# Optimization experiments

Hardware: AMD Instinct MI355X
Metric: run time of the kernel (lower is better)

Reference implementation:

```python
import jax, jax.numpy as jnp
import numpy as np

BUCKET = 64      # bucket_size
N_HASHES = 8
HEADS = 8
EMB = 256
DH = EMB // HEADS  # 32, per-head dim
SELF_ATTN_VAL = -5e4  # TOKEN_SELF_ATTN_VALUE in reformer-pytorch


def haar_dwt2_per(x):
    # one-level 2D haar DWT, periodization mode. x: [B,C,H,W] (H,W even)
    B, C, H, W = x.shape
    x = x.reshape(B, C, H // 2, 2, W // 2, 2)
    a = x[:, :, :, 0, :, 0]
    b = x[:, :, :, 0, :, 1]
    c = x[:, :, :, 1, :, 0]
    d = x[:, :, :, 1, :, 1]
    ll = (a + b + c + d) * 0.5
    lh = (a - b + c - d) * 0.5  # high-pass along W
    hl = (a + b - c - d) * 0.5  # high-pass along H
    hh = (a - b - c + d) * 0.5
    return ll, lh, hl, hh


def maxpool_3s2p1(x):
    # MaxPool2d(kernel=3, stride=2, padding=1)
    return jax.lax.reduce_window(x, -jnp.inf, jax.lax.max,
                                 (1, 1, 3, 3), (1, 1, 2, 2),
                                 ((0, 0), (0, 0), (1, 1), (1, 1)))


def _look_one_back(a):
    # concat each chunk with the previous chunk (wrap-around), along axis 2
    prev = jnp.concatenate([a[:, -1:], a[:, :-1]], axis=1)
    return jnp.concatenate([a, prev], axis=2)


def lsh_attention(qk, v, rotations):
    # qk, v: [bh, t, d]; rotations: [d, n_hashes, n_buckets//2]
    bh, t, d = qk.shape
    n_buckets = t // BUCKET
    # --- hash ---
    rotated = jnp.einsum('btf,fhi->bhti', qk, rotations)        # [bh,nh,t,nb/2]
    rotated = jnp.concatenate([rotated, -rotated], axis=-1)     # [bh,nh,t,nb]
    buckets = jnp.argmax(rotated, axis=-1)                      # [bh,nh,t]
    offsets = (jnp.arange(N_HASHES) * n_buckets)[None, :, None]
    buckets = (buckets + offsets).reshape(bh, -1)               # [bh, nh*t]
    # --- sort tokens by bucket ---
    ticker = jnp.arange(N_HASHES * t)
    bat = t * buckets + (ticker % t)[None, :]
    sticker = jnp.argsort(bat, axis=-1)                         # stable sort
    undo = jnp.argsort(sticker, axis=-1)
    st = sticker % t
    sqk = jnp.take_along_axis(qk, st[..., None], axis=1)
    sv = jnp.take_along_axis(v, st[..., None], axis=1)
    nc = N_HASHES * n_buckets
    bq_t = st.reshape(bh, nc, BUCKET)
    bqk = sqk.reshape(bh, nc, BUCKET, d)
    bv = sv.reshape(bh, nc, BUCKET, d)
    bq = bqk
    norm = jnp.linalg.norm(bqk, axis=-1, keepdims=True)
    bk = bqk / jnp.maximum(norm, 1e-6)                          # make_unit_length
    bk = _look_one_back(bk)
    bv = _look_one_back(bv)
    bkv_t = _look_one_back(bq_t[..., None])[..., 0]
    # --- bucketed attention ---
    dots = jnp.einsum('bnie,bnje->bnij', bq, bk) * (d ** -0.5)  # [bh,nc,64,128]
    self_mask = bq_t[:, :, :, None] == bkv_t[:, :, None, :]
    dots = jnp.where(self_mask, SELF_ATTN_VAL, dots)
    lse = jax.scipy.special.logsumexp(dots, axis=-1, keepdims=True)
    probs = jnp.exp(dots - lse)
    bo = jnp.einsum('bnij,bnje->bnie', probs, bv)
    so = bo.reshape(bh, -1, d)
    slog = lse.reshape(bh, -1)
    # --- unsort and combine hash rounds ---
    o = jnp.take_along_axis(so, undo[..., None], axis=1).reshape(bh, N_HASHES, t, d)
    logits = jnp.take_along_axis(slog, undo, axis=1).reshape(bh, N_HASHES, t, 1)
    w = jnp.exp(logits - jax.scipy.special.logsumexp(logits, axis=1, keepdims=True))
    return jnp.sum(o * w, axis=1)                               # [bh, t, d]


def setup_inputs() -> dict:
    key = jax.random.key(0)
    ks = jax.random.split(key, 6)
    B, C, H, W = 16, 128, 32, 32
    scale = 1.0 / np.sqrt(EMB)
    return {
        'x': jax.random.normal(ks[0], (B, C, H, W), dtype=jnp.float32),
        'w_qk': jax.random.normal(ks[1], (EMB, EMB), dtype=jnp.float32) * scale,
        'w_v': jax.random.normal(ks[2], (EMB, EMB), dtype=jnp.float32) * scale,
        'w_out': jax.random.normal(ks[3], (EMB, EMB), dtype=jnp.float32) * scale,
        'b_out': jnp.zeros((EMB,), dtype=jnp.float32),
        'rotations': jax.random.normal(ks[4], (DH, N_HASHES, 5), dtype=jnp.float32),
    }


def reference(x, w_qk, w_v, w_out, b_out, rotations):
    B = x.shape[0]
    x_spatial = maxpool_3s2p1(x)                      # [B,C,16,16]
    ll, lh, hl, hh = haar_dwt2_per(x)                 # each [B,C,16,16]
    xc = jnp.concatenate([x_spatial, ll, lh, hl, hh], axis=1)  # [B,5C,16,16]
    _, N, Hh, Ww = xc.shape
    tokens = xc.reshape(B, N, Hh * Ww)                # [B, 640, 256]
    qk = tokens @ w_qk
    v = tokens @ w_v
    qkh = qk.reshape(B, N, HEADS, DH).transpose(0, 2, 1, 3).reshape(B * HEADS, N, DH)
    vh = v.reshape(B, N, HEADS, DH).transpose(0, 2, 1, 3).reshape(B * HEADS, N, DH)
    o = lsh_attention(qkh, vh, rotations)
    o = o.reshape(B, HEADS, N, DH).transpose(0, 2, 1, 3).reshape(B, N, EMB)
    out = o @ w_out + b_out
    return out.reshape(B, N, Hh, Ww)
```

## Files before the change

### kernel.cpp

```cpp
#include <hip/hip_runtime.h>
#include <math.h>

#define B_     16
#define CIN_   128
#define NTOK_  640
#define PSP_   256
#define EMB_   256
#define HEADS_ 8
#define DH_    32
#define BH_    128
#define NH_    8
#define NBK_   10
#define NC_    80
#define TOTROWS_ 10240
#define SORTLEN_ 5120
#define VSTRIDE 136
#define OCSTR  264

typedef __attribute__((ext_vector_type(8))) short short8;
typedef __attribute__((ext_vector_type(4))) short short4v;
typedef __attribute__((ext_vector_type(4))) float f32x4;

__device__ __forceinline__ unsigned bf16r(float f) {
  return (__float_as_uint(f) + 0x8000u) >> 16;
}

__device__ __forceinline__ unsigned cvt_pk_bf16(float a, float b) {
  unsigned r;
  asm("v_cvt_pk_bf16_f32 %0, %1, %2" : "=v"(r) : "v"(a), "v"(b));
  return r;
}

__global__ __launch_bounds__(256) void k_tokens(const float* __restrict__ x,
                                                float* __restrict__ tok,
                                                const float* __restrict__ wv,
                                                const float* __restrict__ wo,
                                                unsigned short* __restrict__ wtv,
                                                unsigned short* __restrict__ wto) {
  if (blockIdx.x < 256) {
    int idx = blockIdx.x * 256 + threadIdx.x;
    int n = idx >> 8, k = idx & 255;
    wtv[idx] = (unsigned short)bf16r(wv[k * 256 + n]);
    wto[idx] = (unsigned short)bf16r(wo[k * 256 + n]);
  }
  int tid = blockIdx.x * 256 + threadIdx.x;
  int p  = tid & 255;
  int bc = tid >> 8;
  int i = p >> 4, j = p & 15;
  const float* xp = x + (size_t)bc * 1024;
  int r0 = i * 2, c0 = j * 2;

  float mx = -3.4e38f;
  #pragma unroll
  for (int dr = -1; dr <= 1; dr++) {
    int r = r0 + dr;
    if (r < 0 || r >= 32) continue;
    #pragma unroll
    for (int dc = -1; dc <= 1; dc++) {
      int cc = c0 + dc;
      if (cc < 0 || cc >= 32) continue;
      mx = fmaxf(mx, xp[r * 32 + cc]);
    }
  }
  float a  = xp[r0 * 32 + c0];
  float bv = xp[r0 * 32 + c0 + 1];
  float cv = xp[(r0 + 1) * 32 + c0];
  float dv = xp[(r0 + 1) * 32 + c0 + 1];
  float ll = (a + bv + cv + dv) * 0.5f;
  float lh = (a - bv + cv - dv) * 0.5f;
  float hl = (a + bv - cv - dv) * 0.5f;
  float hh = (a - bv - cv + dv) * 0.5f;

  int b = bc >> 7, c = bc & 127;
  float* tb = tok + (size_t)b * NTOK_ * PSP_ + p;
  tb[(size_t)(c      ) * PSP_] = mx;
  tb[(size_t)(c + 128) * PSP_] = ll;
  tb[(size_t)(c + 256) * PSP_] = lh;
  tb[(size_t)(c + 384) * PSP_] = hl;
  tb[(size_t)(c + 512) * PSP_] = hh;
}

__global__ __launch_bounds__(256) void k_gemm_qv(const float* __restrict__ A,
                                                 const float* __restrict__ Wq,
                                                 const unsigned short* __restrict__ WTv,
                                                 float* __restrict__ C,
                                                 unsigned short* __restrict__ Cb,
                                                 unsigned short* __restrict__ Cv) {
  __shared__ float As[64][68];
  __shared__ float Bs[64][64];
  int tid = threadIdx.x;

  if (blockIdx.x < 640) {
    int bx = blockIdx.x;
    int row0 = (bx >> 2) * 64, col0 = (bx & 3) * 64;
    int tx = tid & 15, ty = tid >> 4;
    float acc[4][4] = {};

    int lrow = tid >> 2, lkq = tid & 3;
    int bkr = tid >> 4, bcq = tid & 15;

    for (int k0 = 0; k0 < 256; k0 += 64) {
      float4 va[4], vb4[4];
      #pragma unroll
      for (int i = 0; i < 4; i++) {
        va[i]  = *(const float4*)(&A[(size_t)(row0 + lrow) * 256 + k0 + i * 16 + 4 * lkq]);
        vb4[i] = *(const float4*)(&Wq[(size_t)(k0 + i * 16 + bkr) * 256 + col0 + 4 * bcq]);
      }
      __syncthreads();
      #pragma unroll
      for (int i = 0; i < 4; i++) {
        As[i * 16 + 4 * lkq + 0][lrow] = va[i].x;
        As[i * 16 + 4 * lkq + 1][lrow] = va[i].y;
        As[i * 16 + 4 * lkq + 2][lrow] = va[i].z;
        As[i * 16 + 4 * lkq + 3][lrow] = va[i].w;
        *(float4*)(&Bs[i * 16 + bkr][4 * bcq]) = vb4[i];
      }
      __syncthreads();
      #pragma unroll
      for (int k = 0; k < 64; k++) {
        const float4 b4 = *(const float4*)(&Bs[k][4 * tx]);
        const float4 a4 = *(const float4*)(&As[k][4 * ty]);
        float ar[4] = {a4.x, a4.y, a4.z, a4.w};
        #pragma unroll
        for (int r = 0; r < 4; r++) {
          acc[r][0] += ar[r] * b4.x; acc[r][1] += ar[r] * b4.y;
          acc[r][2] += ar[r] * b4.z; acc[r][3] += ar[r] * b4.w;
        }
      }
    }
    #pragma unroll
    for (int r = 0; r < 4; r++) {
      float4 o;
      o.x = acc[r][0]; o.y = acc[r][1]; o.z = acc[r][2]; o.w = acc[r][3];
      size_t off = (size_t)(row0 + 4 * ty + r) * 256 + col0 + 4 * tx;
      *(float4*)(&C[off]) = o;
      uint2 ub;
      ub.x = bf16r(o.x) | (bf16r(o.y) << 16);
      ub.y = bf16r(o.z) | (bf16r(o.w) << 16);
      *(uint2*)(&Cb[off]) = ub;
    }
  } else {
    int vbk = blockIdx.x - 640;
    int wid = tid >> 6, lane = tid & 63;
    int lane15 = lane & 15, quad = lane >> 4;
    int row0 = (vbk >> 1) * 64 + wid * 16;
    int col0 = (vbk & 1) * 128;

    short8 fa[8];
    const float* arow = A + (size_t)(row0 + lane15) * 256;
    #pragma unroll
    for (int kc = 0; kc < 8; kc++) {
      float4 x0 = *(const float4*)(arow + kc * 32 + quad * 8);
      float4 x1 = *(const float4*)(arow + kc * 32 + quad * 8 + 4);
      short8 f;
      f[0] = (short)bf16r(x0.x); f[1] = (short)bf16r(x0.y);
      f[2] = (short)bf16r(x0.z); f[3] = (short)bf16r(x0.w);
      f[4] = (short)bf16r(x1.x); f[5] = (short)bf16r(x1.y);
      f[6] = (short)bf16r(x1.z); f[7] = (short)bf16r(x1.w);
      fa[kc] = f;
    }
    #pragma unroll
    for (int nt = 0; nt < 8; nt++) {
      int col = col0 + nt * 16 + lane15;
      f32x4 acc = {0.f, 0.f, 0.f, 0.f};
      const unsigned short* wrow = WTv + (size_t)col * 256;
      #pragma unroll
      for (int kc = 0; kc < 8; kc++) {
        short8 fb = *(const short8*)(wrow + kc * 32 + quad * 8);
        acc = __builtin_amdgcn_mfma_f32_16x16x32_bf16(fa[kc], fb, acc, 0, 0, 0);
      }
      #pragma unroll
      for (int rg = 0; rg < 4; rg++)
        Cv[(size_t)(row0 + 4 * quad + rg) * 256 + col] = (unsigned short)bf16r(acc[rg]);
    }
  }
}

__global__ __launch_bounds__(640) void k_sort(const float* __restrict__ qkg,
                                              const float* __restrict__ rot,
                                              int* __restrict__ st,
                                              float* __restrict__ nrmv) {
  int h = blockIdx.x, bh = blockIdx.y;
  int b = bh >> 3, head = bh & 7;
  __shared__ float srot[5][32];
  __shared__ int wcnt[10][10];
  __shared__ int woff[10][10];
  __shared__ int gbase[10];
  int tid = threadIdx.x, wv = tid >> 6, ln = tid & 63;

  if (tid < 160) {
    int i = tid >> 5, f = tid & 31;
    srot[i][f] = rot[f * (NH_ * 5) + h * 5 + i];
  }
  __syncthreads();

  int t = tid;
  const float* qr = qkg + ((size_t)b * NTOK_ + t) * EMB_ + head * DH_;
  float q[32];
  #pragma unroll
  for (int d4 = 0; d4 < 8; d4++) {
    float4 f = *(const float4*)(qr + d4 * 4);
    q[d4 * 4 + 0] = f.x; q[d4 * 4 + 1] = f.y; q[d4 * 4 + 2] = f.z; q[d4 * 4 + 3] = f.w;
  }
  if (h == 0) {
    float d2 = 0.f;
    #pragma unroll
    for (int dd = 0; dd < 32; dd++) d2 += q[dd] * q[dd];
    nrmv[(size_t)bh * NTOK_ + t] = sqrtf(d2);
  }
  float r[5];
  #pragma unroll
  for (int i = 0; i < 5; i++) {
    float d = 0.f;
    #pragma unroll
    for (int dd = 0; dd < 32; dd++) d += q[dd] * srot[i][dd];
    r[i] = d;
  }
  int bi = 0; float best = r[0];
  #pragma unroll
  for (int i = 1; i < 5; i++) if (r[i] > best) { best = r[i]; bi = i; }
  #pragma unroll
  for (int i = 0; i < 5; i++) if (-r[i] > best) { best = -r[i]; bi = 5 + i; }

  int myoff = 0;
  #pragma unroll
  for (int kb = 0; kb < 10; kb++) {
    unsigned long long mask = __ballot(bi == kb);
    if (ln == 0) wcnt[wv][kb] = (int)__popcll(mask);
    if (bi == kb) myoff = (int)__popcll(mask & ((1ull << ln) - 1ull));
  }
  __syncthreads();
  if (tid < 10) {
    int run = 0;
    #pragma unroll
    for (int w2 = 0; w2 < 10; w2++) { int tmp = wcnt[w2][tid]; woff[w2][tid] = run; run += tmp; }
    gbase[tid] = run;
  }
  __syncthreads();
  if (tid == 0) {
    int run = 0;
    #pragma unroll
    for (int kb = 0; kb < 10; kb++) { int tmp = gbase[kb]; gbase[kb] = run; run += tmp; }
  }
  __syncthreads();
  int rank = gbase[bi] + woff[wv][bi] + myoff;
  size_t gb = (size_t)bh * SORTLEN_ + (size_t)h * 640;
  st[gb + rank] = t;
}

__global__ __launch_bounds__(256) void k_attn(const unsigned short* __restrict__ qkb,
                                              const unsigned short* __restrict__ vb,
                                              const int* __restrict__ st,
                                              const float* __restrict__ nrmv,
                                              unsigned short* __restrict__ osort,
                                              float* __restrict__ lseg) {
  __shared__ __attribute__((aligned(16))) short sK[4096];
  __shared__ __attribute__((aligned(16))) short sVT[32 * VSTRIDE];
  __shared__ __attribute__((aligned(16))) short sP[2048];
  __shared__ float sM[64];
  __shared__ float sIK[128];
  __shared__ float sL[64];
  __shared__ int   stkv[128];

  const float scale = 0.17677669529663687f;
  const float LOG2E = 1.4426950408889634f;
  const float K2 = scale * LOG2E;
  int c = blockIdx.x, bh = blockIdx.y;
  int b = bh >> 3, head = bh & 7;
  int lane = threadIdx.x & 63, wid = threadIdx.x >> 6;
  size_t stb = (size_t)bh * SORTLEN_;
  int pcv = (c + NC_ - 1) % NC_;

  {
    int slot = threadIdx.x & 127;
    int hf   = threadIdx.x >> 7;
    int p0 = (slot < 64) ? (c * 64 + slot) : (pcv * 64 + (slot - 64));
    int t0 = st[stb + p0];
    size_t rowoff = ((size_t)(b * NTOK_ + t0)) * EMB_ + head * DH_;

    const uint4* kr = (const uint4*)(qkb + rowoff);
    uint4 ka = kr[2 * hf], kb2 = kr[2 * hf + 1];
    int pr = slot >> 1;
    int blk0 = ((slot & 1) << 2) | (2 * hf);
    *(uint4*)(&sK[pr * 64 + (((blk0    ) ^ (pr & 7)) << 3)]) = ka;
    *(uint4*)(&sK[pr * 64 + (((blk0 + 1) ^ (pr & 7)) << 3)]) = kb2;
    if (hf == 0) {
      stkv[slot] = t0;
      float nr = nrmv[(size_t)bh * NTOK_ + t0];
      if (slot < 64) sM[slot] = nr * scale;
      sIK[slot] = K2 / fmaxf(nr, 1e-6f);
    }

    const uint4* vr = (const uint4*)(vb + rowoff);
    uint4 va = vr[2 * hf], vb4 = vr[2 * hf + 1];
    unsigned uw[8] = {va.x, va.y, va.z, va.w, vb4.x, vb4.y, vb4.z, vb4.w};
    int vslot = (slot & 96) | (((slot & 15) >> 2) << 3) | (((slot >> 4) & 1) << 2) | (slot & 3);
    short* vbase = &sVT[hf * 16 * VSTRIDE + vslot];
    #pragma unroll
    for (int j = 0; j < 16; j++) {
      unsigned s = (j & 1) ? (uw[j >> 1] >> 16) : uw[j >> 1];
      vbase[j * VSTRIDE] = (short)s;
    }
  }
  __syncthreads();

  int lane15 = lane & 15, quad = lane >> 4;

  short8 fall[8];
  #pragma unroll
  for (int i = 0; i < 8; i++) {
    int key = 16 * i + lane15, pr = key >> 1;
    int blk = ((key & 1) << 2) | quad;
    fall[i] = *(const short8*)(&sK[pr * 64 + ((blk ^ (pr & 7)) << 3)]);
  }
  short8 fq;
  {
    int row = 16 * wid + lane15, pr = row >> 1;
    int blk = ((row & 1) << 2) | quad;
    fq = *(const short8*)(&sK[pr * 64 + ((blk ^ (pr & 7)) << 3)]);
  }

  int   tq  = stkv[16 * wid + lane15];
  float mq  = sM[16 * wid + lane15];
  float mq2 = mq * LOG2E;

  f32x4 O[2];
  #pragma unroll
  for (int vt = 0; vt < 2; vt++) { O[vt][0]=0.f; O[vt][1]=0.f; O[vt][2]=0.f; O[vt][3]=0.f; }
  float lacc = 0.f;

  #pragma unroll
  for (int s = 0; s < 4; s++) {
    f32x4 z = {0.f, 0.f, 0.f, 0.f};
    f32x4 Sv[2];
    #pragma unroll
    for (int ct = 0; ct < 2; ct++)
      Sv[ct] = __builtin_amdgcn_mfma_f32_16x16x32_bf16(fall[2 * s + ct], fq, z, 0, 0, 0);

    unsigned pk[2][2];
    #pragma unroll
    for (int ct = 0; ct < 2; ct++) {
      const int4   k4 = *(const int4*)(&stkv[32 * s + 16 * ct + 4 * quad]);
      const float4 c4 = *(const float4*)(&sIK[32 * s + 16 * ct + 4 * quad]);
      int   kk[4] = {k4.x, k4.y, k4.z, k4.w};
      float cc[4] = {c4.x, c4.y, c4.z, c4.w};
      float e[4];
      #pragma unroll
      for (int rg = 0; rg < 4; rg++) {
        float v = __builtin_exp2f(__builtin_fmaf(Sv[ct][rg], cc[rg], -mq2));
        if (kk[rg] == tq) v = 0.f;
        lacc += v;
        e[rg] = v;
      }
      pk[ct][0] = cvt_pk_bf16(e[0], e[1]);
      pk[ct][1] = cvt_pk_bf16(e[2], e[3]);
    }
    short8 fp;
    {
      union { unsigned u[4]; short8 v; } cv_;
      cv_.u[0] = pk[0][0]; cv_.u[1] = pk[0][1];
      cv_.u[2] = pk[1][0]; cv_.u[3] = pk[1][1];
      fp = cv_.v;
    }
    short8 fv[2];
    #pragma unroll
    for (int vt = 0; vt < 2; vt++)
      fv[vt] = *(const short8*)(&sVT[(16 * vt + lane15) * VSTRIDE + 32 * s + (quad << 3)]);
    #pragma unroll
    for (int vt = 0; vt < 2; vt++)
      O[vt] = __builtin_amdgcn_mfma_f32_16x16x32_bf16(fp, fv[vt], O[vt], 0, 0, 0);
  }

  lacc += __shfl_xor(lacc, 16);
  lacc += __shfl_xor(lacc, 32);

  int h = c / NBK_;
  if (lane < 16) {
    sL[16 * wid + lane] = lacc;
    lseg[((size_t)bh * NTOK_ + tq) * NH_ + h] = mq + __logf(lacc);
  }
  float4 lr = *(const float4*)(&sL[16 * wid + 4 * quad]);
  float lrow[4] = {lr.x, lr.y, lr.z, lr.w};
  #pragma unroll
  for (int rg = 0; rg < 4; rg++) {
    float invl = 1.f / lrow[rg];
    #pragma unroll
    for (int vt = 0; vt < 2; vt++) {
      float o = O[vt][rg] * invl;
      sP[(16 * wid + 4 * quad + rg) * 32 + 16 * vt + lane15] = (short)bf16r(o);
    }
  }
  __syncthreads();
  {
    int row = threadIdx.x >> 2, seg = threadIdx.x & 3;
    int t = stkv[row];
    uint4* dst = (uint4*)(osort + (((size_t)bh * NTOK_ + t) * NH_ + h) * 32 + seg * 8);
    *dst = ((const uint4*)sP)[threadIdx.x];
  }
}

__global__ __launch_bounds__(256) void k_combine_gemm(const unsigned short* __restrict__ osort,
                                                      const float* __restrict__ lseg,
                                                      const unsigned short* __restrict__ WT,
                                                      const float* __restrict__ bias,
                                                      float* __restrict__ C) {
  __shared__ __attribute__((aligned(16))) short sOC[32 * OCSTR];
  int bid = blockIdx.x;
  int b = bid / 20, rt = bid % 20;
  int t0 = rt * 32;
  int tid = threadIdx.x;

  {
    int tk = tid & 31, head = tid >> 5;
    int bh = b * 8 + head;
    size_t base = (size_t)bh * NTOK_ + (t0 + tk);
    float l[8];
    float4 l0 = *(const float4*)(lseg + base * 8);
    float4 l1 = *(const float4*)(lseg + base * 8 + 4);
    l[0]=l0.x; l[1]=l0.y; l[2]=l0.z; l[3]=l0.w;
    l[4]=l1.x; l[5]=l1.y; l[6]=l1.z; l[7]=l1.w;
    float m = -3.4e38f;
    #pragma unroll
    for (int h = 0; h < 8; h++) m = fmaxf(m, l[h]);
    float ssum = 0.f;
    #pragma unroll
    for (int h = 0; h < 8; h++) { l[h] = __expf(l[h] - m); ssum += l[h]; }
    float inv = 1.0f / ssum;
    float acc[32] = {};
    const uint4* orows = (const uint4*)(osort + base * 256);
    #pragma unroll
    for (int h = 0; h < 8; h++) {
      float w = l[h] * inv;
      #pragma unroll
      for (int blk = 0; blk < 4; blk++) {
        uint4 u = orows[h * 4 + blk];
        unsigned uu[4] = {u.x, u.y, u.z, u.w};
        #pragma unroll
        for (int q2 = 0; q2 < 4; q2++) {
          float lo = __uint_as_float(uu[q2] << 16);
          float hi = __uint_as_float(uu[q2] & 0xFFFF0000u);
          acc[blk * 8 + q2 * 2 + 0] += w * lo;
          acc[blk * 8 + q2 * 2 + 1] += w * hi;
        }
      }
    }
    short* dst = &sOC[tk * OCSTR + head * 32];
    #pragma unroll
    for (int q4 = 0; q4 < 4; q4++) {
      uint4 u;
      u.x = bf16r(acc[q4 * 8 + 0]) | (bf16r(acc[q4 * 8 + 1]) << 16);
      u.y = bf16r(acc[q4 * 8 + 2]) | (bf16r(acc[q4 * 8 + 3]) << 16);
      u.z = bf16r(acc[q4 * 8 + 4]) | (bf16r(acc[q4 * 8 + 5]) << 16);
      u.w = bf16r(acc[q4 * 8 + 6]) | (bf16r(acc[q4 * 8 + 7]) << 16);
      *(uint4*)(dst + q4 * 8) = u;
    }
  }
  __syncthreads();

  int wid = tid >> 6, lane = tid & 63;
  int lane15 = lane & 15, quad = lane >> 4;
  int rowt = wid & 1, colh = wid >> 1;
  int lrow0 = rowt * 16;
  int col0 = colh * 128;

  short8 fa[8];
  const short* arow = &sOC[(lrow0 + lane15) * OCSTR];
  #pragma unroll
  for (int kc = 0; kc < 8; kc++)
    fa[kc] = *(const short8*)(arow + kc * 32 + quad * 8);
  #pragma unroll
  for (int nt = 0; nt < 8; nt++) {
    int col = col0 + nt * 16 + lane15;
    f32x4 acc = {0.f, 0.f, 0.f, 0.f};
    const unsigned short* wrow = WT + (size_t)col * 256;
    #pragma unroll
    for (int kc = 0; kc < 8; kc++) {
      short8 fb = *(const short8*)(wrow + kc * 32 + quad * 8);
      acc = __builtin_amdgcn_mfma_f32_16x16x32_bf16(fa[kc], fb, acc, 0, 0, 0);
    }
    float bb = bias[col];
    #pragma unroll
    for (int rg = 0; rg < 4; rg++)
      C[(size_t)(b * NTOK_ + t0 + lrow0 + 4 * quad + rg) * 256 + col] = acc[rg] + bb;
  }
}

extern "C" void kernel_launch(void* const* d_in, const int* in_sizes, int n_in,
                              void* d_out, int out_size, void* d_ws, size_t ws_size,
                              hipStream_t stream) {
  const float* x     = (const float*)d_in[0];
  const float* w_qk  = (const float*)d_in[1];
  const float* w_v   = (const float*)d_in[2];
  const float* w_out = (const float*)d_in[3];
  const float* b_out = (const float*)d_in[4];
  const float* rot   = (const float*)d_in[5];
  float* out = (float*)d_out;

  float* tokens  = (float*)d_ws;
  float* qk      = tokens + 2621440;
  unsigned short* qkb = (unsigned short*)(qk + 2621440);
  unsigned short* vbv = qkb + 2621440;
  int*   st      = (int*)(vbv + 2621440);
  float* lse     = (float*)(st + 655360);
  unsigned short* osort = (unsigned short*)(lse + 655360);
  unsigned short* wtv = osort + 20971520;
  unsigned short* wto = wtv + 65536;
  float* nrmv = tokens;

  k_tokens<<<2048, 256, 0, stream>>>(x, tokens, w_v, w_out, wtv, wto);
  k_gemm_qv<<<960, 256, 0, stream>>>(tokens, w_qk, wtv, qk, qkb, vbv);
  k_sort<<<dim3(8, 128), 640, 0, stream>>>(qk, rot, st, nrmv);
  k_attn<<<dim3(80, 128), 256, 0, stream>>>(qkb, vbv, st, nrmv, osort, lse);
  k_combine_gemm<<<320, 256, 0, stream>>>(osort, lse, wto, b_out, out);
}
```

Baseline: 205.3 us.

## Split combine and output projection into separate kernels with finer parallelism

The fused combine+GEMM kernel, which ran 320 blocks with each thread reading a full 512-byte osort row, is split in two. A combine kernel uses 4 threads per token with 16-byte loads across 1280 blocks and writes a bf16 combined buffer to global memory. A separate projection kernel then does the MFMA GEMM over 640 blocks of 16 rows. The aim is more parallelism and better-coalesced loads in the memory-bound combine step, at the cost of an extra launch and a global round trip for the intermediate buffer.

```diff
diff --git a/kernel.cpp b/kernel.cpp
--- a/kernel.cpp
+++ b/kernel.cpp
@@ -15,7 +15,6 @@
 #define TOTROWS_ 10240
 #define SORTLEN_ 5120
 #define VSTRIDE 136
-#define OCSTR  264
 
 typedef __attribute__((ext_vector_type(8))) short short8;
 typedef __attribute__((ext_vector_type(4))) short short4v;
@@ -399,77 +398,72 @@
   }
 }
 
-__global__ __launch_bounds__(256) void k_combine_gemm(const unsigned short* __restrict__ osort,
-                                                      const float* __restrict__ lseg,
-                                                      const unsigned short* __restrict__ WT,
-                                                      const float* __restrict__ bias,
-                                                      float* __restrict__ C) {
-  __shared__ __attribute__((aligned(16))) short sOC[32 * OCSTR];
-  int bid = blockIdx.x;
-  int b = bid / 20, rt = bid % 20;
-  int t0 = rt * 32;
+__global__ __launch_bounds__(256) void k_combine(const unsigned short* __restrict__ osort,
+                                                 const float* __restrict__ lseg,
+                                                 unsigned short* __restrict__ cmb) {
+  int g = blockIdx.x * 256 + threadIdx.x;
+  int part = g & 3;
+  int task = g >> 2;
+  int bh = task / 640;
+  int t  = task - bh * 640;
+  size_t base = (size_t)task;
+
+  float l[8];
+  float4 l0 = *(const float4*)(lseg + base * 8);
+  float4 l1 = *(const float4*)(lseg + base * 8 + 4);
+  l[0]=l0.x; l[1]=l0.y; l[2]=l0.z; l[3]=l0.w;
+  l[4]=l1.x; l[5]=l1.y; l[6]=l1.z; l[7]=l1.w;
+  float m = -3.4e38f;
+  #pragma unroll
+  for (int h = 0; h < 8; h++) m = fmaxf(m, l[h]);
+  float ssum = 0.f;
+  #pragma unroll
+  for (int h = 0; h < 8; h++) { l[h] = __expf(l[h] - m); ssum += l[h]; }
+  float inv = 1.0f / ssum;
+
+  float acc[8] = {};
+  const uint4* orows = (const uint4*)osort;
+  size_t obase = base * 32 + part;
+  #pragma unroll
+  for (int h = 0; h < 8; h++) {
+    float w = l[h] * inv;
+    uint4 u = orows[obase + h * 4];
+    unsigned uu[4] = {u.x, u.y, u.z, u.w};
+    #pragma unroll
+    for (int q2 = 0; q2 < 4; q2++) {
+      float lo = __uint_as_float(uu[q2] << 16);
+      float hi = __uint_as_float(uu[q2] & 0xFFFF0000u);
+      acc[q2 * 2 + 0] += w * lo;
+      acc[q2 * 2 + 1] += w * hi;
+    }
+  }
+  int b = bh >> 3, head = bh & 7;
+  uint4 o;
+  o.x = bf16r(acc[0]) | (bf16r(acc[1]) << 16);
+  o.y = bf16r(acc[2]) | (bf16r(acc[3]) << 16);
+  o.z = bf16r(acc[4]) | (bf16r(acc[5]) << 16);
+  o.w = bf16r(acc[6]) | (bf16r(acc[7]) << 16);
+  *(uint4*)(cmb + ((size_t)(b * NTOK_ + t)) * 256 + head * 32 + part * 8) = o;
+}
+
+__global__ __launch_bounds__(256) void k_oproj(const unsigned short* __restrict__ cmb,
+                                               const unsigned short* __restrict__ WT,
+                                               const float* __restrict__ bias,
+                                               float* __restrict__ C) {
+  int rt = blockIdx.x;
   int tid = threadIdx.x;
-
-  {
-    int tk = tid & 31, head = tid >> 5;
-    int bh = b * 8 + head;
-    size_t base = (size_t)bh * NTOK_ + (t0 + tk);
-    float l[8];
-    float4 l0 = *(const float4*)(lseg + base * 8);
-    float4 l1 = *(const float4*)(lseg + base * 8 + 4);
-    l[0]=l0.x; l[1]=l0.y; l[2]=l0.z; l[3]=l0.w;
-    l[4]=l1.x; l[5]=l1.y; l[6]=l1.z; l[7]=l1.w;
-    float m = -3.4e38f;
-    #pragma unroll
-    for (int h = 0; h < 8; h++) m = fmaxf(m, l[h]);
-    float ssum = 0.f;
-    #pragma unroll
-    for (int h = 0; h < 8; h++) { l[h] = __expf(l[h] - m); ssum += l[h]; }
-    float inv = 1.0f / ssum;
-    float acc[32] = {};
-    const uint4* orows = (const uint4*)(osort + base * 256);
-    #pragma unroll
-    for (int h = 0; h < 8; h++) {
-      float w = l[h] * inv;
-      #pragma unroll
-      for (int blk = 0; blk < 4; blk++) {
-        uint4 u = orows[h * 4 + blk];
-        unsigned uu[4] = {u.x, u.y, u.z, u.w};
-        #pragma unroll
-        for (int q2 = 0; q2 < 4; q2++) {
-          float lo = __uint_as_float(uu[q2] << 16);
-          float hi = __uint_as_float(uu[q2] & 0xFFFF0000u);
-          acc[blk * 8 + q2 * 2 + 0] += w * lo;
-          acc[blk * 8 + q2 * 2 + 1] += w * hi;
-        }
-      }
-    }
-    short* dst = &sOC[tk * OCSTR + head * 32];
-    #pragma unroll
-    for (int q4 = 0; q4 < 4; q4++) {
-      uint4 u;
-      u.x = bf16r(acc[q4 * 8 + 0]) | (bf16r(acc[q4 * 8 + 1]) << 16);
-      u.y = bf16r(acc[q4 * 8 + 2]) | (bf16r(acc[q4 * 8 + 3]) << 16);
-      u.z = bf16r(acc[q4 * 8 + 4]) | (bf16r(acc[q4 * 8 + 5]) << 16);
-      u.w = bf16r(acc[q4 * 8 + 6]) | (bf16r(acc[q4 * 8 + 7]) << 16);
-      *(uint4*)(dst + q4 * 8) = u;
-    }
-  }
-  __syncthreads();
-
   int wid = tid >> 6, lane = tid & 63;
   int lane15 = lane & 15, quad = lane >> 4;
-  int rowt = wid & 1, colh = wid >> 1;
-  int lrow0 = rowt * 16;
-  int col0 = colh * 128;
+  int row0 = rt * 16;
+  int col0 = wid * 64;
 
   short8 fa[8];
-  const short* arow = &sOC[(lrow0 + lane15) * OCSTR];
+  const unsigned short* arow = cmb + (size_t)(row0 + lane15) * 256;
   #pragma unroll
   for (int kc = 0; kc < 8; kc++)
     fa[kc] = *(const short8*)(arow + kc * 32 + quad * 8);
   #pragma unroll
-  for (int nt = 0; nt < 8; nt++) {
+  for (int nt = 0; nt < 4; nt++) {
     int col = col0 + nt * 16 + lane15;
     f32x4 acc = {0.f, 0.f, 0.f, 0.f};
     const unsigned short* wrow = WT + (size_t)col * 256;
@@ -481,7 +475,7 @@
     float bb = bias[col];
     #pragma unroll
     for (int rg = 0; rg < 4; rg++)
-      C[(size_t)(b * NTOK_ + t0 + lrow0 + 4 * quad + rg) * 256 + col] = acc[rg] + bb;
+      C[(size_t)(row0 + 4 * quad + rg) * 256 + col] = acc[rg] + bb;
   }
 }
 
@@ -506,10 +500,12 @@
   unsigned short* wtv = osort + 20971520;
   unsigned short* wto = wtv + 65536;
   float* nrmv = tokens;
+  unsigned short* cmb = (unsigned short*)qk;
 
   k_tokens<<<2048, 256, 0, stream>>>(x, tokens, w_v, w_out, wtv, wto);
   k_gemm_qv<<<960, 256, 0, stream>>>(tokens, w_qk, wtv, qk, qkb, vbv);
   k_sort<<<dim3(8, 128), 640, 0, stream>>>(qk, rot, st, nrmv);
   k_attn<<<dim3(80, 128), 256, 0, stream>>>(qkb, vbv, st, nrmv, osort, lse);
-  k_combine_gemm<<<320, 256, 0, stream>>>(osort, lse, wto, b_out, out);
-}
+  k_combine<<<1280, 256, 0, stream>>>(osort, lse, cmb);
+  k_oproj<<<640, 256, 0, stream>>>(cmb, wto, b_out, out);
+}
```

After: 199.4 us. -2.9%, faster.
